# Performance work log

Measured on AMD Instinct MI355X. Metric: run time of the kernel, lower is better.

Reference implementation:

```python
import jax, jax.numpy as jnp
import numpy as np

Q_UPPER = 64  # number of quantization bins for upper-layer distributions
CLIP_LO, CLIP_HI = 1e-15, 1e15


def setup_inputs() -> dict:
    key = jax.random.key(0)
    k = jax.random.split(key, 6)
    B, NU, NL, QU, QL = 256, 64, 64, Q_UPPER, 64
    w_init = 0.1
    P = jax.random.uniform(k[0], (B, NL, QL), dtype=jnp.float32)
    weight = jax.random.uniform(k[1], (NU, NL), minval=-w_init, maxval=w_init, dtype=jnp.float32)
    bias_abs = jax.random.uniform(k[2], (NU, 1), minval=-w_init, maxval=w_init, dtype=jnp.float32)
    bias_q = jax.random.uniform(k[3], (NU, 1), minval=-w_init, maxval=w_init, dtype=jnp.float32)
    lambda_abs = jax.random.uniform(k[4], (NU, 1), minval=0.0, maxval=1.0, dtype=jnp.float32)
    lambda_q = jax.random.uniform(k[5], (NU, 1), minval=0.0, maxval=1.0, dtype=jnp.float32)
    return {"P": P, "weight": weight, "bias_abs": bias_abs, "bias_q": bias_q,
            "lambda_abs": lambda_abs, "lambda_q": lambda_q}


def reference(P, weight, bias_abs, bias_q, lambda_abs, lambda_q):
    # P: [B, n_lower, q_lower]; weight: [n_upper, n_lower]; biases/lambdas: [n_upper, 1]
    QU = Q_UPPER
    QL = P.shape[2]
    s1 = jnp.arange(QU, dtype=P.dtype) / QU          # upper bin centers
    s0 = jnp.arange(QL, dtype=P.dtype) / QL          # lower bin centers
    diff2 = (s0[None, :] - s1[:, None]) ** 2          # [QU, QL]
    # D = exp(-diff2); T = D**weight = exp(-weight * diff2), permuted to [NU, NL, QU, QL]
    T = jnp.exp(-weight[:, :, None, None] * diff2[None, None, :, :])
    # batched GEMV over q_lower: Pw[i,j,k,l] = sum_m T[j,k,l,m] * P[i,k,m]
    Pw = jnp.einsum('jklm,ikm->ijkl', T, P)           # [B, NU, NL, QU]
    logPw = jnp.log(jnp.clip(Pw, CLIP_LO, CLIP_HI))
    logsum = jnp.sum(logPw, axis=2)                   # [B, NU, QU]
    sq = jnp.arange(QU, dtype=P.dtype)[None, :] / QU  # [1, QU]
    exponent_B = (-bias_q * (sq - lambda_q) ** 2
                  - bias_abs * jnp.abs(sq - lambda_abs))  # [NU, QU]
    logsumB = logsum + exponent_B[None, :, :]
    return jax.nn.softmax(logsumB, axis=2)            # [B, NU, QU]
```

## Files before the change

### kernel.cpp

```cpp
#include <hip/hip_runtime.h>


#define NUP 64
#define NLOW 64
#define QUP 64
#define QLOW 64

__global__ __launch_bounds__(512, 4)
void drn_kernel(const float* __restrict__ P,
                const float* __restrict__ weight,
                const float* __restrict__ bias_abs,
                const float* __restrict__ bias_q,
                const float* __restrict__ lambda_abs,
                const float* __restrict__ lambda_q,
                float* __restrict__ out)
{
    __shared__ float lds_mom[NLOW * 12];
    __shared__ float lds_m12[NLOW * QUP * 2];
    __shared__ float lds_m34[NLOW * QUP * 2];
    __shared__ float lds_wT[NLOW * 36];

    const int i    = blockIdx.x >> 1;
    const int jh   = blockIdx.x & 1;
    const int tid  = threadIdx.x;
    const int lane = tid & 63;
    const int wv   = tid >> 6;

    {
        const int j  = tid >> 4;
        const int k0 = (tid & 15) * 4;
        const float4 w4 = *reinterpret_cast<const float4*>(
            weight + (size_t)(jh * 32 + j) * NLOW + k0);
        lds_wT[(k0 + 0) * 36 + j] = w4.x;
        lds_wT[(k0 + 1) * 36 + j] = w4.y;
        lds_wT[(k0 + 2) * 36 + j] = w4.z;
        lds_wT[(k0 + 3) * 36 + j] = w4.w;
    }

    {
        const int kk = lane >> 3;
        const int mc = lane & 7;
        const int k  = wv * 8 + kk;
        const float* Pr = P + ((size_t)i * NLOW + k) * QLOW + mc * 8;
        const float4 pa = *reinterpret_cast<const float4*>(Pr);
        const float4 pb = *reinterpret_cast<const float4*>(Pr + 4);

        float t0 = 0.f, t1 = 0.f, t2 = 0.f, t3 = 0.f, t4 = 0.f,
              t5 = 0.f, t6 = 0.f, t7 = 0.f, t8 = 0.f;
        const float s0 = (float)(mc * 8) * 0.015625f;
#define ACCM(PV, S) { float f = (PV); const float s_ = (S); \
        t0 += f; f *= s_; t1 += f; f *= s_; t2 += f; f *= s_; t3 += f; f *= s_; \
        t4 += f; f *= s_; t5 += f; f *= s_; t6 += f; f *= s_; t7 += f; f *= s_; t8 += f; }
        ACCM(pa.x, s0);
        ACCM(pa.y, s0 + 0.015625f);
        ACCM(pa.z, s0 + 0.03125f);
        ACCM(pa.w, s0 + 0.046875f);
        ACCM(pb.x, s0 + 0.0625f);
        ACCM(pb.y, s0 + 0.078125f);
        ACCM(pb.z, s0 + 0.09375f);
        ACCM(pb.w, s0 + 0.109375f);
#undef ACCM
#define RED9(OFF) { t0 += __shfl_xor(t0, OFF, 64); t1 += __shfl_xor(t1, OFF, 64); \
        t2 += __shfl_xor(t2, OFF, 64); t3 += __shfl_xor(t3, OFF, 64); \
        t4 += __shfl_xor(t4, OFF, 64); t5 += __shfl_xor(t5, OFF, 64); \
        t6 += __shfl_xor(t6, OFF, 64); t7 += __shfl_xor(t7, OFF, 64); \
        t8 += __shfl_xor(t8, OFF, 64); }
        RED9(1) RED9(2) RED9(4)
#undef RED9
        if (mc == 0) {
            float* mp = &lds_mom[k * 12];
            *reinterpret_cast<float4*>(mp)     = make_float4(t0, t1, t2, t3);
            *reinterpret_cast<float4*>(mp + 4) = make_float4(t4, t5, t6, t7);
            mp[8] = t8;
        }
    }
    __syncthreads();

    const float s1l = (float)lane * 0.015625f;
    {
        const float z  = -s1l;
        const float z2 = z * z, z3 = z2 * z, z4 = z2 * z2;
        const float z5 = z4 * z, z6 = z4 * z2, z7 = z6 * z, z8 = z4 * z4;
        const float c10 = z2,               c11 = 2.f * z;
        const float c20 = 0.5f * z4,        c21 = 2.f * z3,        c22 = 3.f * z2,
                    c23 = 2.f * z;
        const float c30 = z6 * (1.f / 6.f), c31 = z5,              c32 = 2.5f * z4,
                    c33 = (10.f / 3.f) * z3, c34 = 2.5f * z2,      c35 = z;
        const float c40 = z8 * (1.f / 24.f), c41 = z7 * (1.f / 3.f), c42 = (7.f / 6.f) * z6,
                    c43 = (7.f / 3.f) * z5, c44 = (35.f / 12.f) * z4, c45 = (7.f / 3.f) * z3,
                    c46 = (7.f / 6.f) * z2, c47 = z * (1.f / 3.f);

#pragma unroll
        for (int kk = 0; kk < 8; ++kk) {
            const int k = wv * 8 + kk;
            const float4 q0 = *reinterpret_cast<const float4*>(&lds_mom[k * 12]);
            const float4 q1 = *reinterpret_cast<const float4*>(&lds_mom[k * 12 + 4]);
            const float  q8 = lds_mom[k * 12 + 8];

            const float m1 = fmaf(c10, q0.x, fmaf(c11, q0.y, q0.z));
            const float m2 = fmaf(c20, q0.x, fmaf(c21, q0.y, fmaf(c22, q0.z,
                             fmaf(c23, q0.w, 0.5f * q1.x))));
            const float m3 = fmaf(c30, q0.x, fmaf(c31, q0.y, fmaf(c32, q0.z,
                             fmaf(c33, q0.w, fmaf(c34, q1.x, fmaf(c35, q1.y,
                             (1.f / 6.f) * q1.z))))));
            const float m4 = fmaf(c40, q0.x, fmaf(c41, q0.y, fmaf(c42, q0.z,
                             fmaf(c43, q0.w, fmaf(c44, q1.x, fmaf(c45, q1.y,
                             fmaf(c46, q1.z, fmaf(c47, q1.w, (1.f / 24.f) * q8))))))));

            *reinterpret_cast<float2*>(&lds_m12[(k * QUP + lane) * 2]) = make_float2(m1, m2);
            *reinterpret_cast<float2*>(&lds_m34[(k * QUP + lane) * 2]) = make_float2(m3, m4);
        }
    }
    __syncthreads();

    float acc0 = 0.f, acc1 = 0.f, acc2 = 0.f, acc3 = 0.f;
    for (int k8 = 0; k8 < 8; ++k8) {
        float pr0 = 1.f, pr1 = 1.f, pr2 = 1.f, pr3 = 1.f;
#pragma unroll
        for (int kk = 0; kk < 8; ++kk) {
            const int k = k8 * 8 + kk;
            const float4 w4  = *reinterpret_cast<const float4*>(&lds_wT[k * 36 + wv * 4]);
            const float  m0  = lds_mom[k * 12];
            const float2 v12 = *reinterpret_cast<const float2*>(&lds_m12[(k * QUP + lane) * 2]);
            const float2 v34 = *reinterpret_cast<const float2*>(&lds_m34[(k * QUP + lane) * 2]);
#define STEPJ(W, PR) { float t = fmaf(-(W), v34.y, v34.x); \
            t = fmaf(-(W), t, v12.y); t = fmaf(-(W), t, v12.x); \
            t = fmaf(-(W), t, m0); PR *= fmaxf(t, 1e-15f); }
            STEPJ(w4.x, pr0)
            STEPJ(w4.y, pr1)
            STEPJ(w4.z, pr2)
            STEPJ(w4.w, pr3)
#undef STEPJ
        }
        acc0 += __log2f(pr0);
        acc1 += __log2f(pr1);
        acc2 += __log2f(pr2);
        acc3 += __log2f(pr3);
    }

    const float LOG2E = 1.4426950408889634f;
    auto finish = [&](float a, int jj) {
        const int j = jh * 32 + wv * 4 + jj;
        const float dq = s1l - lambda_q[j];
        float y = fmaf(-bias_q[j] * LOG2E, dq * dq, a);
        y = fmaf(-bias_abs[j] * LOG2E, fabsf(s1l - lambda_abs[j]), y);
        float mx = y;
#pragma unroll
        for (int off = 32; off >= 1; off >>= 1)
            mx = fmaxf(mx, __shfl_xor(mx, off, 64));
        const float e = exp2f(y - mx);
        float s = e;
#pragma unroll
        for (int off = 32; off >= 1; off >>= 1)
            s += __shfl_xor(s, off, 64);
        out[((size_t)i * NUP + j) * QUP + lane] = e / s;
    };
    finish(acc0, 0);
    finish(acc1, 1);
    finish(acc2, 2);
    finish(acc3, 3);
}

extern "C" void kernel_launch(void* const* d_in, const int* in_sizes, int n_in,
                              void* d_out, int out_size, void* d_ws, size_t ws_size,
                              hipStream_t stream) {
    const float* P          = (const float*)d_in[0];
    const float* weight     = (const float*)d_in[1];
    const float* bias_abs   = (const float*)d_in[2];
    const float* bias_q     = (const float*)d_in[3];
    const float* lambda_abs = (const float*)d_in[4];
    const float* lambda_q   = (const float*)d_in[5];
    (void)in_sizes; (void)n_in; (void)out_size; (void)d_ws; (void)ws_size;

    drn_kernel<<<dim3(512), dim3(512), 0, stream>>>(
        P, weight, bias_abs, bias_q, lambda_abs, lambda_q, (float*)d_out);
}
```

Baseline: 82.02 us.

## Normalize moments by mass, pack into float4 LDS, take one log per row

Divides each lower node's Taylor moments by its zeroth moment and stores the four ratios as one float4 per (k,lane) in LDS. Because m0 does not depend on the upper bin, the dropped factor cancels in the softmax, so the inner loop can multiply terms near 1. That removes the clamp, the m0 load and the seven extra log2 calls per row. Weights are now read straight from global memory through wave-uniform pointers, likely as scalar loads, which replaces the transposed weight tile in LDS. The risk is that without the clamp, a negative or zero term or underflow in the 64-term product goes unguarded, which changes numerics in edge cases.

```diff
diff --git a/kernel.cpp b/kernel.cpp
--- a/kernel.cpp
+++ b/kernel.cpp
@@ -15,27 +15,14 @@
                 const float* __restrict__ lambda_q,
                 float* __restrict__ out)
 {
-    __shared__ float lds_mom[NLOW * 12];
-    __shared__ float lds_m12[NLOW * QUP * 2];
-    __shared__ float lds_m34[NLOW * QUP * 2];
-    __shared__ float lds_wT[NLOW * 36];
+    __shared__ float  lds_mom[NLOW * 12];
+    __shared__ float4 lds_n[NLOW * QUP];
 
     const int i    = blockIdx.x >> 1;
     const int jh   = blockIdx.x & 1;
     const int tid  = threadIdx.x;
     const int lane = tid & 63;
-    const int wv   = tid >> 6;
-
-    {
-        const int j  = tid >> 4;
-        const int k0 = (tid & 15) * 4;
-        const float4 w4 = *reinterpret_cast<const float4*>(
-            weight + (size_t)(jh * 32 + j) * NLOW + k0);
-        lds_wT[(k0 + 0) * 36 + j] = w4.x;
-        lds_wT[(k0 + 1) * 36 + j] = w4.y;
-        lds_wT[(k0 + 2) * 36 + j] = w4.z;
-        lds_wT[(k0 + 3) * 36 + j] = w4.w;
-    }
+    const int wv   = __builtin_amdgcn_readfirstlane(tid >> 6);
 
     {
         const int kk = lane >> 3;
@@ -81,14 +68,14 @@
         const float z  = -s1l;
         const float z2 = z * z, z3 = z2 * z, z4 = z2 * z2;
         const float z5 = z4 * z, z6 = z4 * z2, z7 = z6 * z, z8 = z4 * z4;
-        const float c10 = z2,               c11 = 2.f * z;
-        const float c20 = 0.5f * z4,        c21 = 2.f * z3,        c22 = 3.f * z2,
+        const float c10 = z2,                c11 = 2.f * z;
+        const float c20 = 0.5f * z4,         c21 = 2.f * z3,          c22 = 3.f * z2,
                     c23 = 2.f * z;
-        const float c30 = z6 * (1.f / 6.f), c31 = z5,              c32 = 2.5f * z4,
-                    c33 = (10.f / 3.f) * z3, c34 = 2.5f * z2,      c35 = z;
-        const float c40 = z8 * (1.f / 24.f), c41 = z7 * (1.f / 3.f), c42 = (7.f / 6.f) * z6,
-                    c43 = (7.f / 3.f) * z5, c44 = (35.f / 12.f) * z4, c45 = (7.f / 3.f) * z3,
-                    c46 = (7.f / 6.f) * z2, c47 = z * (1.f / 3.f);
+        const float c30 = z6 * (1.f / 6.f),  c31 = z5,                c32 = 2.5f * z4,
+                    c33 = (10.f / 3.f) * z3, c34 = 2.5f * z2,         c35 = z;
+        const float c40 = z8 * (1.f / 24.f), c41 = z7 * (1.f / 3.f),  c42 = (7.f / 6.f) * z6,
+                    c43 = (7.f / 3.f) * z5,  c44 = (35.f / 12.f) * z4, c45 = (7.f / 3.f) * z3,
+                    c46 = (7.f / 6.f) * z2,  c47 = z * (1.f / 3.f);
 
 #pragma unroll
         for (int kk = 0; kk < 8; ++kk) {
@@ -97,6 +84,7 @@
             const float4 q1 = *reinterpret_cast<const float4*>(&lds_mom[k * 12 + 4]);
             const float  q8 = lds_mom[k * 12 + 8];
 
+            const float inv = 1.0f / q0.x;
             const float m1 = fmaf(c10, q0.x, fmaf(c11, q0.y, q0.z));
             const float m2 = fmaf(c20, q0.x, fmaf(c21, q0.y, fmaf(c22, q0.z,
                              fmaf(c23, q0.w, 0.5f * q1.x))));
@@ -107,38 +95,46 @@
                              fmaf(c43, q0.w, fmaf(c44, q1.x, fmaf(c45, q1.y,
                              fmaf(c46, q1.z, fmaf(c47, q1.w, (1.f / 24.f) * q8))))))));
 
-            *reinterpret_cast<float2*>(&lds_m12[(k * QUP + lane) * 2]) = make_float2(m1, m2);
-            *reinterpret_cast<float2*>(&lds_m34[(k * QUP + lane) * 2]) = make_float2(m3, m4);
+            lds_n[k * QUP + lane] = make_float4(m1 * inv, m2 * inv, m3 * inv, m4 * inv);
         }
     }
     __syncthreads();
 
-    float acc0 = 0.f, acc1 = 0.f, acc2 = 0.f, acc3 = 0.f;
+    const float* __restrict__ w0r = weight + (size_t)(jh * 32 + wv * 4 + 0) * NLOW;
+    const float* __restrict__ w1r = weight + (size_t)(jh * 32 + wv * 4 + 1) * NLOW;
+    const float* __restrict__ w2r = weight + (size_t)(jh * 32 + wv * 4 + 2) * NLOW;
+    const float* __restrict__ w3r = weight + (size_t)(jh * 32 + wv * 4 + 3) * NLOW;
+
+    float pr0 = 1.f, pr1 = 1.f, pr2 = 1.f, pr3 = 1.f;
     for (int k8 = 0; k8 < 8; ++k8) {
-        float pr0 = 1.f, pr1 = 1.f, pr2 = 1.f, pr3 = 1.f;
+        float w0[8], w1[8], w2[8], w3[8];
 #pragma unroll
         for (int kk = 0; kk < 8; ++kk) {
-            const int k = k8 * 8 + kk;
-            const float4 w4  = *reinterpret_cast<const float4*>(&lds_wT[k * 36 + wv * 4]);
-            const float  m0  = lds_mom[k * 12];
-            const float2 v12 = *reinterpret_cast<const float2*>(&lds_m12[(k * QUP + lane) * 2]);
-            const float2 v34 = *reinterpret_cast<const float2*>(&lds_m34[(k * QUP + lane) * 2]);
-#define STEPJ(W, PR) { float t = fmaf(-(W), v34.y, v34.x); \
-            t = fmaf(-(W), t, v12.y); t = fmaf(-(W), t, v12.x); \
-            t = fmaf(-(W), t, m0); PR *= fmaxf(t, 1e-15f); }
-            STEPJ(w4.x, pr0)
-            STEPJ(w4.y, pr1)
-            STEPJ(w4.z, pr2)
-            STEPJ(w4.w, pr3)
+            w0[kk] = w0r[k8 * 8 + kk];
+            w1[kk] = w1r[k8 * 8 + kk];
+            w2[kk] = w2r[k8 * 8 + kk];
+            w3[kk] = w3r[k8 * 8 + kk];
+        }
+#pragma unroll
+        for (int kk = 0; kk < 8; ++kk) {
+            const float4 n = lds_n[(k8 * 8 + kk) * QUP + lane];
+#define STEPJ(W, PR) { const float w_ = (W); \
+            float t = fmaf(-w_, n.w, n.z); \
+            t = fmaf(-w_, t, n.y); t = fmaf(-w_, t, n.x); \
+            PR *= fmaf(-w_, t, 1.0f); }
+            STEPJ(w0[kk], pr0)
+            STEPJ(w1[kk], pr1)
+            STEPJ(w2[kk], pr2)
+            STEPJ(w3[kk], pr3)
 #undef STEPJ
         }
-        acc0 += __log2f(pr0);
-        acc1 += __log2f(pr1);
-        acc2 += __log2f(pr2);
-        acc3 += __log2f(pr3);
     }
 
     const float LOG2E = 1.4426950408889634f;
+    const float acc0 = __log2f(pr0);
+    const float acc1 = __log2f(pr1);
+    const float acc2 = __log2f(pr2);
+    const float acc3 = __log2f(pr3);
     auto finish = [&](float a, int jj) {
         const int j = jh * 32 + wv * 4 + jj;
         const float dq = s1l - lambda_q[j];
```

Result: faster. 76.21 us (-7.1%).
